# Optimization experiments

Measured on AMD Instinct MI355X. Metric: run time of the kernel, lower is better.

Reference implementation:

```python
import jax, jax.numpy as jnp
import numpy as np

N = 8192
IN_F = 128
OUT_F = 128
ALPHA = 0.2  # LeakyReLU negative slope
NEG_INF = -9e15


def setup_inputs() -> dict:
    key = jax.random.key(0)
    k1, k2, k3, k4, k5 = jax.random.split(key, 5)
    mole_out = jax.random.normal(k1, (N, IN_F), dtype=jnp.float32)
    adj = jax.random.randint(k2, (N, N), 0, 2, dtype=jnp.int32)
    # nn.Linear(in_features, out_features, bias=False): y = x @ W  (W stored as [in, out])
    W = jax.random.normal(k3, (IN_F, OUT_F), dtype=jnp.float32) / np.sqrt(IN_F)
    # nn.Linear(2*out_features, 1, bias=False) weight split into a1 (for Wh_i) and a2 (for Wh_j)
    a1 = jax.random.normal(k4, (OUT_F,), dtype=jnp.float32) / np.sqrt(2 * OUT_F)
    a2 = jax.random.normal(k5, (OUT_F,), dtype=jnp.float32) / np.sqrt(2 * OUT_F)
    return {"mole_out": mole_out, "adj": adj, "W": W, "a1": a1, "a2": a2}


def reference(mole_out, adj, W, a1, a2):
    Wh = mole_out @ W                       # (N, F)
    # a([Wh_i || Wh_j]) = a1.Wh_i + a2.Wh_j  -- avoids the O(N^2*2F) concat tensor
    s1 = Wh @ a1                            # (N,)
    s2 = Wh @ a2                            # (N,)
    e = jax.nn.leaky_relu(s1[:, None] + s2[None, :], negative_slope=ALPHA)  # (N, N)
    att = jnp.where(adj > 0, e, NEG_INF)
    att = jax.nn.softmax(att, axis=1)       # row softmax over neighbors j
    # dropout_gnn = 0.0 -> identity
    h_prime = att @ Wh                      # (N, F)
    return jax.nn.elu(h_prime)              # concat=True branch
```

## Files before the change

kernel.cpp:

```cpp
#include <hip/hip_runtime.h>
#include <hip/hip_bf16.h>

#define NROW 8192
#define NF   128
#define LOG2E 1.4426950408889634f

typedef float f32x4  __attribute__((ext_vector_type(4)));
typedef int   i32x4  __attribute__((ext_vector_type(4)));
typedef short bf16x8 __attribute__((ext_vector_type(8)));
typedef short bf16x4 __attribute__((ext_vector_type(4)));
typedef unsigned long long u64;

__device__ __forceinline__ short f2bf(float f) {
    union { float f; unsigned u; } v; v.f = f;
    unsigned r = v.u + 0x7FFFu + ((v.u >> 16) & 1u);
    return (short)(r >> 16);
}

__device__ __forceinline__ void gload_lds16(const short* g, short* l) {
    __builtin_amdgcn_global_load_lds(
        (const __attribute__((address_space(1))) void*)g,
        (__attribute__((address_space(3))) void*)l, 16, 0, 0);
}


__global__ __launch_bounds__(256) void k0_wt(const float* __restrict__ W,
                                             short* __restrict__ WT) {
    int idx = blockIdx.x * 256 + threadIdx.x;
    int c = idx >> 7, k = idx & 127;
    WT[c * NF + k] = f2bf(W[k * NF + c]);
}

__global__ __launch_bounds__(256) void k1_wh(const float* __restrict__ mo,
        const short* __restrict__ WT,
        const float* __restrict__ a1, const float* __restrict__ a2,
        short* __restrict__ WhT, float* __restrict__ s1g, float* __restrict__ s2g) {
    __shared__ float s_lds[2][32];
    int t = threadIdx.x;
    int w = t >> 6, l = t & 63, lg = l >> 4, lr = l & 15;
    int rows0 = blockIdx.x * 32;
    if (t < 64) s_lds[t >> 5][t & 31] = 0.0f;
    __syncthreads();

    f32x4 acc[2][2] = {};
#pragma unroll
    for (int ks = 0; ks < 4; ++ks) {
        bf16x8 a[2], b[2];
#pragma unroll
        for (int rt = 0; rt < 2; ++rt) {
            const float* ap = mo + (size_t)(rows0 + rt*16 + lr) * NF + ks*32 + lg*8;
            f32x4 x0 = *(const f32x4*)ap;
            f32x4 x1 = *(const f32x4*)(ap + 4);
#pragma unroll
            for (int e = 0; e < 4; ++e) { a[rt][e] = f2bf(x0[e]); a[rt][4+e] = f2bf(x1[e]); }
        }
#pragma unroll
        for (int ct = 0; ct < 2; ++ct) {
            int c = w*32 + ct*16 + lr;
            b[ct] = *(const bf16x8*)(WT + c*NF + ks*32 + lg*8);
        }
#pragma unroll
        for (int rt = 0; rt < 2; ++rt)
#pragma unroll
            for (int ct = 0; ct < 2; ++ct)
                acc[rt][ct] = __builtin_amdgcn_mfma_f32_16x16x32_bf16(a[rt], b[ct], acc[rt][ct], 0, 0, 0);
    }

#pragma unroll
    for (int rt = 0; rt < 2; ++rt) {
        float p1[4] = {0,0,0,0}, p2[4] = {0,0,0,0};
#pragma unroll
        for (int ct = 0; ct < 2; ++ct) {
            int c = w*32 + ct*16 + lr;
            float a1c = a1[c], a2c = a2[c];
            bf16x4 wv;
#pragma unroll
            for (int g = 0; g < 4; ++g) {
                float v = acc[rt][ct][g];
                wv[g] = f2bf(v);
                p1[g] += v * a1c;
                p2[g] += v * a2c;
            }
            int r0 = rows0 + rt*16 + lg*4;
            size_t off = (size_t)(r0 >> 6) * 8192 + (size_t)(c >> 4) * 1024
                       + (size_t)((r0 >> 5) & 1) * 512 + (size_t)((r0 >> 3) & 3) * 128
                       + (size_t)(c & 15) * 8 + (size_t)(r0 & 7);
            *(bf16x4*)(WhT + off) = wv;
        }
#pragma unroll
        for (int off = 1; off < 16; off <<= 1) {
#pragma unroll
            for (int g = 0; g < 4; ++g) {
                p1[g] += __shfl_xor(p1[g], off);
                p2[g] += __shfl_xor(p2[g], off);
            }
        }
        if (lr == 0) {
            int rloc = rt*16 + lg*4;
#pragma unroll
            for (int g = 0; g < 4; ++g) {
                atomicAdd(&s_lds[0][rloc+g], p1[g]);
                atomicAdd(&s_lds[1][rloc+g], p2[g]);
            }
        }
    }
    __syncthreads();
    if (t < 32)       s1g[rows0 + t]        = s_lds[0][t] * LOG2E;
    else if (t < 64)  s2g[rows0 + (t - 32)] = s_lds[1][t - 32] * LOG2E;
}

__global__ __launch_bounds__(256, 4) void k2_main(
        const int* __restrict__ adj, const short* __restrict__ WhT,
        const float* __restrict__ s1g, const float* __restrict__ s2g,
        float* __restrict__ numP, float* __restrict__ zP,
        int S, int npb) {
    __shared__ __attribute__((aligned(16))) short Bl[2][8192];
    __shared__ __attribute__((aligned(16))) float s2l[2048];

    int t = threadIdx.x, w = t >> 6, l = t & 63;
    int lo = l & 15, hi = l >> 4;
    int b = blockIdx.x, jseg = b % S, rg = b / S;
    int wrows0 = (rg << 6) + (w << 4);
    int j0 = jseg * npb;
    int NT = npb >> 6;

    for (int i = t; i < (npb >> 2); i += 256)
        ((f32x4*)s2l)[i] = ((const f32x4*)(s2g + j0))[i];

    float s1v = s1g[wrows0 + lo];
    const int* arow = adj + (size_t)wrows0 * NROW + j0 + l;

    f32x4 acc[8] = {};
    float z = 0.0f;

    int An[16];
#pragma unroll
    for (int r = 0; r < 16; ++r) An[r] = arow[r * NROW];
    {
        const short* gs = WhT + (size_t)(j0 >> 6) * 8192 + w*2048 + l*8;
        short* ds = &Bl[0][w*2048];
#pragma unroll
        for (int r4 = 0; r4 < 4; ++r4)
            gload_lds16(gs + r4*512, ds + r4*512);
    }

    int cur = 0;
    for (int it = 0; it < NT; ++it) {
        __syncthreads();
        u64 bmq = 0;
        int more = (it + 1 < NT);
#pragma unroll
        for (int r = 0; r < 16; ++r) {
            u64 br = __ballot(An[r] > 0);
            if (more) An[r] = arow[r * NROW + ((it + 1) << 6)];
            bmq = (lo == r) ? br : bmq;
        }
        if (more) {
            const short* gs = WhT + (size_t)((j0 + ((it+1) << 6)) >> 6) * 8192 + w*2048 + l*8;
            short* ds = &Bl[cur ^ 1][w*2048];
#pragma unroll
            for (int r4 = 0; r4 < 4; ++r4)
                gload_lds16(gs + r4*512, ds + r4*512);
        }
        int jt = it << 6;
        unsigned blo = (unsigned)(bmq >> (hi * 8)) & 0xffu;
        unsigned bhi = (unsigned)(bmq >> (32 + hi * 8)) & 0xffu;
        f32x4 sa = *(const f32x4*)(s2l + jt + hi*8);
        f32x4 sb = *(const f32x4*)(s2l + jt + hi*8 + 4);
        f32x4 sc = *(const f32x4*)(s2l + jt + 32 + hi*8);
        f32x4 sd = *(const f32x4*)(s2l + jt + 32 + hi*8 + 4);
        float p0[8], p1[8];
#pragma unroll
        for (int e = 0; e < 4; ++e) {
            float x, p;
            x = s1v + sa[e]; p = exp2f(fmaxf(x, 0.2f * x));
            p0[e]   = ((blo >> e) & 1) ? p : 0.0f;      z += p0[e];
            x = s1v + sb[e]; p = exp2f(fmaxf(x, 0.2f * x));
            p0[4+e] = ((blo >> (4+e)) & 1) ? p : 0.0f;  z += p0[4+e];
            x = s1v + sc[e]; p = exp2f(fmaxf(x, 0.2f * x));
            p1[e]   = ((bhi >> e) & 1) ? p : 0.0f;      z += p1[e];
            x = s1v + sd[e]; p = exp2f(fmaxf(x, 0.2f * x));
            p1[4+e] = ((bhi >> (4+e)) & 1) ? p : 0.0f;  z += p1[4+e];
        }
        union { bf16x8 v8; __hip_bfloat162 h2[4]; } fa0u, fa1u;
#pragma unroll
        for (int q = 0; q < 4; ++q) {
            fa0u.h2[q] = __float22bfloat162_rn(make_float2(p0[2*q], p0[2*q+1]));
            fa1u.h2[q] = __float22bfloat162_rn(make_float2(p1[2*q], p1[2*q+1]));
        }
        const short* Bc = &Bl[cur][l * 8];
#pragma unroll
        for (int ct = 0; ct < 8; ++ct) {
            bf16x8 b0 = *(const bf16x8*)(Bc + ct*1024);
            bf16x8 b1 = *(const bf16x8*)(Bc + ct*1024 + 512);
            acc[ct] = __builtin_amdgcn_mfma_f32_16x16x32_bf16(fa0u.v8, b0, acc[ct], 0, 0, 0);
            acc[ct] = __builtin_amdgcn_mfma_f32_16x16x32_bf16(fa1u.v8, b1, acc[ct], 0, 0, 0);
        }
        cur ^= 1;
    }

    z += __shfl_xor(z, 16);
    z += __shfl_xor(z, 32);
    if (l < 16) zP[(size_t)jseg * NROW + wrows0 + lo] = z;

    size_t obase = (size_t)jseg * NROW * NF;
#pragma unroll
    for (int ct = 0; ct < 8; ++ct) {
        int cc = ct * 16 + lo;
        int r0 = wrows0 + hi * 4;
#pragma unroll
        for (int g = 0; g < 4; ++g)
            numP[obase + (size_t)(r0 + g) * NF + cc] = acc[ct][g];
    }
}

__global__ __launch_bounds__(256) void k3_reduce(const float* __restrict__ numP,
        const float* __restrict__ zP, float* __restrict__ out, int S) {
    int idx = (blockIdx.x * 256 + threadIdx.x) * 4;
    int r = idx >> 7;
    f32x4 num = {};
    float zz = 0.0f;
    for (int s = 0; s < S; ++s) {
        f32x4 v = *(const f32x4*)(numP + (size_t)s * (NROW * NF) + idx);
        num += v;
        zz  += zP[s * NROW + r];
    }
    f32x4 o;
#pragma unroll
    for (int e = 0; e < 4; ++e) {
        float h = num[e] / zz;
        o[e] = (h > 0.0f) ? h : expm1f(h);
    }
    *(f32x4*)(out + idx) = o;
}

extern "C" void kernel_launch(void* const* d_in, const int* in_sizes, int n_in,
                              void* d_out, int out_size, void* d_ws, size_t ws_size,
                              hipStream_t stream) {
    const float* mo  = (const float*)d_in[0];
    const int*   adj = (const int*)d_in[1];
    const float* W   = (const float*)d_in[2];
    const float* a1  = (const float*)d_in[3];
    const float* a2  = (const float*)d_in[4];
    float* out = (float*)d_out;

    char* p = (char*)d_ws;
    short* WT  = (short*)p;  p += (size_t)NF * NF * 2;
    short* WhT = (short*)p;  p += (size_t)NF * NROW * 2;
    float* s1  = (float*)p;  p += (size_t)NROW * 4;
    float* s2  = (float*)p;  p += (size_t)NROW * 4;
    float* zP  = (float*)p;  p += (size_t)8 * NROW * 4;
    size_t fixed = (size_t)(p - (char*)d_ws);

    int S = 8;
    while (S > 1 && fixed + (size_t)S * NROW * NF * 4 > ws_size) S >>= 1;
    float* numP = (float*)p;
    if (fixed + (size_t)S * NROW * NF * 4 > ws_size) numP = out;

    k0_wt<<<dim3(64), dim3(256), 0, stream>>>(W, WT);
    k1_wh<<<dim3(256), dim3(256), 0, stream>>>(mo, WT, a1, a2, WhT, s1, s2);
    k2_main<<<dim3((NROW / 64) * S), dim3(256), 0, stream>>>(adj, WhT, s1, s2, numP, zP, S, NROW / S);
    k3_reduce<<<dim3(NROW * NF / 1024), dim3(256), 0, stream>>>(numP, zP, out, S);
}
```

Baseline: 92.40 us.

## Process 128-column tiles per iteration with single LDS buffer instead of double-buffered 64

The main attention kernel now covers 128 neighbor columns per loop iteration, using one 32 KB LDS buffer in place of two 16 KB ping-pong buffers. Adjacency values for both 64-column halves are prefetched into registers. The next WhT tile is loaded into LDS only after the current tile's MFMAs finish, followed by a barrier. This halves the loop-iteration and barrier count, but the LDS load no longer overlaps compute, so each iteration stalls on global-to-LDS latency. Holding twice as many adjacency values in registers may also hurt occupancy.

```diff
diff --git a/kernel.cpp b/kernel.cpp
--- a/kernel.cpp
+++ b/kernel.cpp
@@ -114,7 +114,7 @@
         const float* __restrict__ s1g, const float* __restrict__ s2g,
         float* __restrict__ numP, float* __restrict__ zP,
         int S, int npb) {
-    __shared__ __attribute__((aligned(16))) short Bl[2][8192];
+    __shared__ __attribute__((aligned(16))) short Bl[16384];
     __shared__ __attribute__((aligned(16))) float s2l[2048];
 
     int t = threadIdx.x, w = t >> 6, l = t & 63;
@@ -122,7 +122,7 @@
     int b = blockIdx.x, jseg = b % S, rg = b / S;
     int wrows0 = (rg << 6) + (w << 4);
     int j0 = jseg * npb;
-    int NT = npb >> 6;
+    int NT = npb >> 7;
 
     for (int i = t; i < (npb >> 2); i += 256)
         ((f32x4*)s2l)[i] = ((const f32x4*)(s2g + j0))[i];
@@ -133,70 +133,75 @@
     f32x4 acc[8] = {};
     float z = 0.0f;
 
-    int An[16];
-#pragma unroll
-    for (int r = 0; r < 16; ++r) An[r] = arow[r * NROW];
+    int An[32];
+#pragma unroll
+    for (int r = 0; r < 16; ++r) {
+        An[r]      = arow[r * NROW];
+        An[16 + r] = arow[r * NROW + 64];
+    }
     {
-        const short* gs = WhT + (size_t)(j0 >> 6) * 8192 + w*2048 + l*8;
-        short* ds = &Bl[0][w*2048];
-#pragma unroll
-        for (int r4 = 0; r4 < 4; ++r4)
-            gload_lds16(gs + r4*512, ds + r4*512);
-    }
-
-    int cur = 0;
+        const short* gs = WhT + (size_t)(j0 >> 6) * 8192 + w*4096 + l*8;
+        short* ds = &Bl[w*4096];
+#pragma unroll
+        for (int r8 = 0; r8 < 8; ++r8)
+            gload_lds16(gs + r8*512, ds + r8*512);
+    }
+    __syncthreads();
+
     for (int it = 0; it < NT; ++it) {
+        u64 bmqA = 0, bmqB = 0;
+#pragma unroll
+        for (int r = 0; r < 16; ++r) {
+            u64 brA = __ballot(An[r] > 0);
+            u64 brB = __ballot(An[16 + r] > 0);
+            bmqA = (lo == r) ? brA : bmqA;
+            bmqB = (lo == r) ? brB : bmqB;
+        }
+        int more = (it + 1 < NT);
+        if (more) {
+            int joff = (it + 1) << 7;
+#pragma unroll
+            for (int r = 0; r < 16; ++r) {
+                An[r]      = arow[r * NROW + joff];
+                An[16 + r] = arow[r * NROW + joff + 64];
+            }
+        }
+#pragma unroll
+        for (int ks = 0; ks < 4; ++ks) {
+            u64 bq = (ks < 2) ? bmqA : bmqB;
+            unsigned bits = (unsigned)(bq >> (((ks & 1) << 5) + hi * 8)) & 0xffu;
+            int js = (it << 7) + ks * 32 + hi * 8;
+            f32x4 sa = *(const f32x4*)(s2l + js);
+            f32x4 sb = *(const f32x4*)(s2l + js + 4);
+            float p[8];
+#pragma unroll
+            for (int e = 0; e < 4; ++e) {
+                float x, pe;
+                x = s1v + sa[e]; pe = exp2f(fmaxf(x, 0.2f * x));
+                p[e]     = ((bits >> e) & 1) ? pe : 0.0f;        z += p[e];
+                x = s1v + sb[e]; pe = exp2f(fmaxf(x, 0.2f * x));
+                p[4 + e] = ((bits >> (4 + e)) & 1) ? pe : 0.0f;  z += p[4 + e];
+            }
+            union { bf16x8 v8; __hip_bfloat162 h2[4]; } fau;
+#pragma unroll
+            for (int q = 0; q < 4; ++q)
+                fau.h2[q] = __float22bfloat162_rn(make_float2(p[2*q], p[2*q + 1]));
+            const short* Bc = &Bl[(ks >> 1) * 8192 + (ks & 1) * 512 + l * 8];
+#pragma unroll
+            for (int ct = 0; ct < 8; ++ct) {
+                bf16x8 bv = *(const bf16x8*)(Bc + ct * 1024);
+                acc[ct] = __builtin_amdgcn_mfma_f32_16x16x32_bf16(fau.v8, bv, acc[ct], 0, 0, 0);
+            }
+        }
         __syncthreads();
-        u64 bmq = 0;
-        int more = (it + 1 < NT);
-#pragma unroll
-        for (int r = 0; r < 16; ++r) {
-            u64 br = __ballot(An[r] > 0);
-            if (more) An[r] = arow[r * NROW + ((it + 1) << 6)];
-            bmq = (lo == r) ? br : bmq;
-        }
         if (more) {
-            const short* gs = WhT + (size_t)((j0 + ((it+1) << 6)) >> 6) * 8192 + w*2048 + l*8;
-            short* ds = &Bl[cur ^ 1][w*2048];
-#pragma unroll
-            for (int r4 = 0; r4 < 4; ++r4)
-                gload_lds16(gs + r4*512, ds + r4*512);
-        }
-        int jt = it << 6;
-        unsigned blo = (unsigned)(bmq >> (hi * 8)) & 0xffu;
-        unsigned bhi = (unsigned)(bmq >> (32 + hi * 8)) & 0xffu;
-        f32x4 sa = *(const f32x4*)(s2l + jt + hi*8);
-        f32x4 sb = *(const f32x4*)(s2l + jt + hi*8 + 4);
-        f32x4 sc = *(const f32x4*)(s2l + jt + 32 + hi*8);
-        f32x4 sd = *(const f32x4*)(s2l + jt + 32 + hi*8 + 4);
-        float p0[8], p1[8];
-#pragma unroll
-        for (int e = 0; e < 4; ++e) {
-            float x, p;
-            x = s1v + sa[e]; p = exp2f(fmaxf(x, 0.2f * x));
-            p0[e]   = ((blo >> e) & 1) ? p : 0.0f;      z += p0[e];
-            x = s1v + sb[e]; p = exp2f(fmaxf(x, 0.2f * x));
-            p0[4+e] = ((blo >> (4+e)) & 1) ? p : 0.0f;  z += p0[4+e];
-            x = s1v + sc[e]; p = exp2f(fmaxf(x, 0.2f * x));
-            p1[e]   = ((bhi >> e) & 1) ? p : 0.0f;      z += p1[e];
-            x = s1v + sd[e]; p = exp2f(fmaxf(x, 0.2f * x));
-            p1[4+e] = ((bhi >> (4+e)) & 1) ? p : 0.0f;  z += p1[4+e];
-        }
-        union { bf16x8 v8; __hip_bfloat162 h2[4]; } fa0u, fa1u;
-#pragma unroll
-        for (int q = 0; q < 4; ++q) {
-            fa0u.h2[q] = __float22bfloat162_rn(make_float2(p0[2*q], p0[2*q+1]));
-            fa1u.h2[q] = __float22bfloat162_rn(make_float2(p1[2*q], p1[2*q+1]));
-        }
-        const short* Bc = &Bl[cur][l * 8];
-#pragma unroll
-        for (int ct = 0; ct < 8; ++ct) {
-            bf16x8 b0 = *(const bf16x8*)(Bc + ct*1024);
-            bf16x8 b1 = *(const bf16x8*)(Bc + ct*1024 + 512);
-            acc[ct] = __builtin_amdgcn_mfma_f32_16x16x32_bf16(fa0u.v8, b0, acc[ct], 0, 0, 0);
-            acc[ct] = __builtin_amdgcn_mfma_f32_16x16x32_bf16(fa1u.v8, b1, acc[ct], 0, 0, 0);
-        }
-        cur ^= 1;
+            const short* gs = WhT + (size_t)((j0 + ((it + 1) << 7)) >> 6) * 8192 + w*4096 + l*8;
+            short* ds = &Bl[w*4096];
+#pragma unroll
+            for (int r8 = 0; r8 < 8; ++r8)
+                gload_lds16(gs + r8*512, ds + r8*512);
+            __syncthreads();
+        }
     }
 
     z += __shfl_xor(z, 16);
```

Measured after the change: 88.14 us. 1.05x faster.
